# Optimization experiments

Hardware: AMD Instinct MI355X
Metric: run time of the kernel (lower is better)

The kernel has to match this reference:

```python
import jax, jax.numpy as jnp
import numpy as np

B, TQ, TK, D, NA = 8, 512, 2048, 1024, 512
H, HD = 16, 64          # n_head, head_dim (D = H*HD)
NE, HID = 4, 32         # n_experts, expert hidden_dim
EPS = 1e-6


def _rmsnorm(x, w):
    return x * jax.lax.rsqrt(jnp.mean(x * x, axis=-1, keepdims=True) + EPS) * w


def setup_inputs() -> dict:
    key = jax.random.key(0)
    ks = jax.random.split(key, 20)
    r = lambda i, shp: jax.random.normal(ks[i], shp, dtype=jnp.float32) * 0.02
    return {
        'q': jax.random.normal(ks[0], (B, TQ, D), dtype=jnp.float32),
        'kv': jax.random.normal(ks[1], (B, TK, D), dtype=jnp.float32),
        'qn_w': jnp.ones((D,), jnp.float32),
        'kva_w': jnp.ones((D,), jnp.float32),
        'kvi_w': jnp.ones((D,), jnp.float32),
        'dn_w': jnp.ones((D,), jnp.float32),
        'fn_w': jnp.ones((D,), jnp.float32),
        'Wq': r(2, (D, D)), 'bq': jnp.zeros((D,), jnp.float32),
        'Wk': r(3, (D, D)), 'bk': jnp.zeros((D,), jnp.float32),
        'Wv': r(4, (D, D)), 'bv': jnp.zeros((D,), jnp.float32),
        'Wo': r(5, (D, D)), 'bo': jnp.zeros((D,), jnp.float32),
        'active_bias': r(6, (D,)),
        'inactive_bias': r(7, (D,)),
        'log_temp': jnp.array(0.0, jnp.float32),
        'gate_attn': jnp.array(0.3, jnp.float32),
        'gate_ffn': jnp.array(0.7, jnp.float32),
        'Wr': r(8, (D, NE)), 'br': jnp.zeros((NE,), jnp.float32),
        'W1': r(9, (NE, D, 2 * HID)), 'b1': jnp.zeros((NE, 2 * HID), jnp.float32),
        'W2': r(10, (NE, HID, D)), 'b2': jnp.zeros((NE, D), jnp.float32),
        'kv_mask': jnp.ones((B, TK), bool),
        'n_actives': NA,
    }


def _forward(q, kv, qn_w, kva_w, kvi_w, dn_w, fn_w,
             Wq, bq, Wk, bk, Wv, bv, Wo, bo,
             active_bias, inactive_bias, log_temp, gate_attn, gate_ffn,
             Wr, br, W1, b1, W2, b2, kv_mask, n_actives):
    Na = int(n_actives)
    Tk = kv.shape[1]
    Ni = Tk - Na
    b, tq, d = q.shape

    # split-normed kv, with active/inactive learned biases injected pre-KV-proj
    kv_a = _rmsnorm(kv[:, :Na], kva_w) + active_bias
    kv_i = _rmsnorm(kv[:, Na:], kvi_w) + inactive_bias
    kv_b = jnp.concatenate([kv_a, kv_i], axis=1)

    qn = _rmsnorm(q, qn_w)
    qp = (qn @ Wq + bq).reshape(b, tq, H, HD).transpose(0, 2, 1, 3)  # (B,H,Tq,hd)
    k = (kv_b @ Wk + bk).reshape(b, Tk, H, HD).transpose(0, 2, 1, 3)
    v = (kv_b @ Wv + bv).reshape(b, Tk, H, HD).transpose(0, 2, 1, 3)

    # torch: q *= 1/sqrt(hd), then SDPA(q/temp, ...) applies another 1/sqrt(hd)
    temp = jnp.clip(jnp.exp(log_temp), 0.1, 10.0)
    scale = 1.0 / (HD * temp)

    def attn(kk, vv):
        logits = jnp.einsum('bhqd,bhkd->bhqk', qp, kk) * scale
        return jnp.einsum('bhqk,bhkd->bhqd', jax.nn.softmax(logits, axis=-1), vv)

    out = attn(k[:, :, :Na], v[:, :, :Na]) / np.sqrt(max(Na, 1)) \
        - attn(k[:, :, Na:], v[:, :, Na:]) / np.sqrt(max(Ni, 1))
    out = out.transpose(0, 2, 1, 3).reshape(b, tq, d)
    delta = _rmsnorm(out @ Wo + bo, dn_w)
    q_new = q + jax.nn.sigmoid(gate_attn) * delta

    # dense soft MoE over normed kv, with query-similarity logit bias
    x = _rmsnorm(kv, fn_w)
    logits = x @ Wr + br                                   # (B,Tk,NE)
    q_vec = jnp.mean(q_new, axis=1, keepdims=True)         # (B,1,D)
    sim = jnp.einsum('bqd,btd->bt', q_vec, x)              # (B,Tk)
    probs = jax.nn.softmax(logits + sim[..., None], axis=-1)

    h = jnp.einsum('btd,edh->bteh', x, W1) + b1            # (B,Tk,NE,2*HID)
    xp, g = h[..., :HID], h[..., HID:]
    act = xp * (g * jax.nn.sigmoid(g))                     # SwiGLU
    eo = jnp.einsum('bteh,ehd->bted', act, W2) + b2        # (B,Tk,NE,D)
    moe_out = jnp.einsum('bte,bted->btd', probs, eo)

    kv_new = kv + jax.nn.sigmoid(gate_ffn) * moe_out
    return q_new, kv_new


def reference(q, kv, qn_w, kva_w, kvi_w, dn_w, fn_w,
              Wq, bq, Wk, bk, Wv, bv, Wo, bo,
              active_bias, inactive_bias, log_temp, gate_attn, gate_ffn,
              Wr, br, W1, b1, W2, b2, kv_mask, n_actives):
    return _forward(q, kv, qn_w, kva_w, kvi_w, dn_w, fn_w,
                    Wq, bq, Wk, bk, Wv, bv, Wo, bo,
                    active_bias, inactive_bias, log_temp, gate_attn, gate_ffn,
                    Wr, br, W1, b1, W2, b2, kv_mask, n_actives)
```

## Files before the change

### kernel.cpp

```cpp
#include <hip/hip_runtime.h>
#include <hip/hip_bf16.h>
#include <stdint.h>


#define B_   8
#define TQ_  512
#define TK_  2048
#define D_   1024
#define H_   16
#define HD_  64
#define NE_  4
#define HID_ 32
#define EPSF 1e-6f
#define LOG2E 1.44269504f

typedef __bf16 bf16_t;
typedef __bf16 bf16x8 __attribute__((ext_vector_type(8)));
typedef __bf16 bf16x4 __attribute__((ext_vector_type(4)));
typedef float  f32x4  __attribute__((ext_vector_type(4)));

typedef __attribute__((address_space(1))) void gvoid_t;
typedef __attribute__((address_space(3))) void lvoid_t;

__device__ __forceinline__ void gld_lds16(const void* g, void* l) {
  __builtin_amdgcn_global_load_lds((gvoid_t*)g, (lvoid_t*)l, 16, 0, 0);
}

struct TP2 { const float* in[2]; bf16_t* out[2]; };

__global__ void transpose_conv2_kernel(TP2 p) {
  __shared__ float tile[32][33];
  const int bz = blockIdx.z;
  const float* in = p.in[bz];
  bf16_t* out = p.out[bz];
  const int rb = blockIdx.y * 32, cb = blockIdx.x * 32;
  const int txi = threadIdx.x, tyi = threadIdx.y;
#pragma unroll
  for (int i = 0; i < 32; i += 8)
    tile[tyi + i][txi] = in[(size_t)(rb + tyi + i) * D_ + cb + txi];
  __syncthreads();
#pragma unroll
  for (int i = 0; i < 32; i += 8)
    out[(size_t)(cb + tyi + i) * D_ + rb + txi] = (bf16_t)tile[txi][tyi + i];
}

__global__ void transpose_fragorder_kernel(TP2 p) {
  __shared__ float tile[32][33];
  const float* in = p.in[blockIdx.z];
  bf16_t* out = p.out[blockIdx.z];
  const int kb0 = blockIdx.y * 32;
  const int nb0 = blockIdx.x * 32;
  const int tx = threadIdx.x, ty = threadIdx.y;
#pragma unroll
  for (int i = 0; i < 32; i += 8)
    tile[ty + i][tx] = in[(size_t)(kb0 + ty + i) * D_ + nb0 + tx];
  __syncthreads();
  const int t = ty * 32 + tx;
  const int n_l = t >> 3;
  const int k_l = (t & 7) * 4;
  const int n = nb0 + n_l;
  const int k = kb0 + k_l;
  const int tile_n = n >> 7, rn = n & 127, hc = rn >> 6, rr = rn & 63;
  const int j = rr >> 4, l15 = rr & 15;
  const int s = k >> 5, lg = (k >> 3) & 3, e = k & 7;
  bf16x4 o;
#pragma unroll
  for (int c = 0; c < 4; ++c) o[c] = (bf16_t)tile[k_l + c][n_l];
  *(bf16x4*)&out[(size_t)tile_n * 131072 + s * 4096 + hc * 2048 +
                 j * 512 + (lg * 16 + l15) * 8 + e] = o;
}

__global__ void transpose_conv_kernel(const float* __restrict__ in, bf16_t* __restrict__ out,
                                      int R, int C, int in_bstride,
                                      int out_rstride, int ob_row, int ob_col) {
  __shared__ float tile[32][33];
  const int bz = blockIdx.z;
  const int rb = blockIdx.y * 32, cb = blockIdx.x * 32;
  const int txi = threadIdx.x, tyi = threadIdx.y;
  const float* inp = in + (size_t)bz * in_bstride;
#pragma unroll
  for (int i = 0; i < 32; i += 8) {
    const int r = rb + tyi + i, c = cb + txi;
    if (r < R && c < C) tile[tyi + i][txi] = inp[(size_t)r * C + c];
  }
  __syncthreads();
#pragma unroll
  for (int i = 0; i < 32; i += 8) {
    const int orow = cb + tyi + i;
    const int ocol = rb + txi;
    if (orow < C && ocol < R)
      out[(size_t)(orow + bz * ob_row) * out_rstride + bz * ob_col + ocol] =
          (bf16_t)tile[txi][tyi + i];
  }
}

__device__ __forceinline__ float block_rsum(float v, float* red) {
  v += __shfl_xor(v, 1);  v += __shfl_xor(v, 2);  v += __shfl_xor(v, 4);
  v += __shfl_xor(v, 8);  v += __shfl_xor(v, 16); v += __shfl_xor(v, 32);
  const int tid = threadIdx.x;
  if ((tid & 63) == 0) red[tid >> 6] = v;
  __syncthreads();
  return red[0] + red[1] + red[2] + red[3];
}

__global__ __launch_bounds__(256)
void rms_kv_kernel(const float* __restrict__ kv, const float* __restrict__ kva_w,
                   const float* __restrict__ kvi_w, const float* __restrict__ fn_w,
                   const float* __restrict__ ab, const float* __restrict__ ib,
                   const int* __restrict__ n_act, const float* __restrict__ Wr,
                   const float* __restrict__ br,
                   bf16_t* __restrict__ kvb, bf16_t* __restrict__ xn,
                   float* __restrict__ probs) {
  __shared__ float red[4];
  __shared__ f32x4 pred[4];
  const int row = blockIdx.x;
  const int t = row & (TK_ - 1);
  const int tid = threadIdx.x;
  const float* src = kv + (size_t)row * D_;
  f32x4 v = ((const f32x4*)src)[tid];
  float ss = v[0]*v[0] + v[1]*v[1] + v[2]*v[2] + v[3]*v[3];
  ss = block_rsum(ss, red);
  const float rs = rsqrtf(ss * (1.0f / D_) + EPSF);
  const int Na = n_act[0];
  const float* wsel = (t < Na) ? kva_w : kvi_w;
  const float* bsel = (t < Na) ? ab : ib;
  const int d = tid * 4;
  f32x4 wv = *(const f32x4*)(wsel + d);
  f32x4 bv = *(const f32x4*)(bsel + d);
  f32x4 fv = *(const f32x4*)(fn_w + d);
  bf16x4 o0, o1;
  f32x4 p4 = {};
#pragma unroll
  for (int c = 0; c < 4; ++c) {
    const float xv = v[c] * rs;
    const float xf = xv * fv[c];
    o0[c] = (bf16_t)(xv * wv[c] + bv[c]);
    o1[c] = (bf16_t)xf;
    const f32x4 w4 = *(const f32x4*)&Wr[(d + c) * 4];
    p4 += w4 * xf;
  }
  {
    const int rl = row & 127, hh = rl >> 6, rr2 = rl & 63;
    const int ii = rr2 >> 4, l15 = rr2 & 15;
    const int s2 = d >> 5, lg2 = (d >> 3) & 3, e2 = d & 7;
    *(bf16x4*)&kvb[(size_t)(row >> 7) * 131072 + s2 * 4096 + hh * 2048 +
                   ii * 512 + (lg2 * 16 + l15) * 8 + e2] = o0;
  }
  *(bf16x4*)&xn[(size_t)row * D_ + d] = o1;
#pragma unroll
  for (int m = 1; m <= 32; m <<= 1) {
    p4[0] += __shfl_xor(p4[0], m); p4[1] += __shfl_xor(p4[1], m);
    p4[2] += __shfl_xor(p4[2], m); p4[3] += __shfl_xor(p4[3], m);
  }
  if ((tid & 63) == 0) pred[tid >> 6] = p4;
  __syncthreads();
  if (tid == 0) {
    f32x4 s = pred[0] + pred[1] + pred[2] + pred[3];
    s[0] += br[0]; s[1] += br[1]; s[2] += br[2]; s[3] += br[3];
    const float mx = fmaxf(fmaxf(s[0], s[1]), fmaxf(s[2], s[3]));
    const float e0 = __expf(s[0] - mx), e1 = __expf(s[1] - mx);
    const float e2 = __expf(s[2] - mx), e3 = __expf(s[3] - mx);
    const float inv = 1.0f / (e0 + e1 + e2 + e3);
    f32x4 pr = { e0 * inv, e1 * inv, e2 * inv, e3 * inv };
    *(f32x4*)&probs[row * 4] = pr;
  }
}

__global__ __launch_bounds__(256)
void rms_q_kernel(const float* __restrict__ q, const float* __restrict__ qn_w,
                  bf16_t* __restrict__ qn) {
  __shared__ float red[4];
  const int row = blockIdx.x;
  const int tid = threadIdx.x;
  const float* src = q + (size_t)row * D_;
  f32x4 v = ((const f32x4*)src)[tid];
  float ss = v[0]*v[0] + v[1]*v[1] + v[2]*v[2] + v[3]*v[3];
  ss = block_rsum(ss, red);
  const float rs = rsqrtf(ss * (1.0f / D_) + EPSF);
  const int d = tid * 4;
  f32x4 wv = *(const f32x4*)(qn_w + d);
  bf16x4 o0;
#pragma unroll
  for (int c = 0; c < 4; ++c) o0[c] = (bf16_t)(v[c] * rs * wv[c]);
  *(bf16x4*)&qn[(size_t)row * D_ + d] = o0;
}

__device__ __forceinline__ int xcd_swz(int bx, int gx) {
  if ((gx & 7) == 0) { const int cpx = gx >> 3; return (bx & 7) * cpx + (bx >> 3); }
  return bx;
}

__global__ __launch_bounds__(256)
void gemm_kv(const bf16_t* __restrict__ A, const bf16_t* __restrict__ Wk,
             const bf16_t* __restrict__ Wv, const float* __restrict__ bk,
             const float* __restrict__ bv, bf16_t* __restrict__ Kout,
             bf16_t* __restrict__ Vt) {
  __shared__ alignas(16) bf16_t lds[3 * 12288];
  const int tid = threadIdx.x;
  const int lane = tid & 63;
  const int w = tid >> 6;
  const int wr = w >> 1, wc = w & 1;
  const int lane15 = lane & 15, lgrp = lane >> 4;

  const int flat = blockIdx.x;
  const int xcd = flat & 7;
  const int local = flat >> 3;
  const int tg = local >> 3;
  const int yy = local & 7;
  const int m0 = (xcd * 16 + tg) * 128;
  const int n0 = yy * 128;

  f32x4 acc_k[4][4] = {};
  f32x4 acc_v[4][4] = {};

  const bf16_t* ga = A  + (size_t)(m0 >> 7) * 131072 + tid * 8;
  const bf16_t* gk = Wk + (size_t)(n0 >> 7) * 131072 + tid * 8;
  const bf16_t* gv = Wv + (size_t)(n0 >> 7) * 131072 + tid * 8;

  auto STAGE = [&](int s) {
    bf16_t* dst = lds + (s % 3) * 12288 + tid * 8;
    const size_t so = (size_t)s * 4096;
    gld_lds16(ga + so,        dst);
    gld_lds16(ga + so + 2048, dst + 2048);
    gld_lds16(gk + so,        dst + 4096);
    gld_lds16(gk + so + 2048, dst + 6144);
    gld_lds16(gv + so,        dst + 8192);
    gld_lds16(gv + so + 2048, dst + 10240);
  };

  STAGE(0);
  STAGE(1);

  const int abase = wr * 2048 + lane * 8;
  const int bbase = wc * 2048 + lane * 8;
  for (int s = 0; s < 32; ++s) {
    if (s < 30) asm volatile("s_waitcnt vmcnt(6)" ::: "memory");
    else        asm volatile("s_waitcnt vmcnt(0)" ::: "memory");
    __builtin_amdgcn_s_barrier();
    __builtin_amdgcn_sched_barrier(0);
    const bf16_t* buf = lds + (s % 3) * 12288;
    bf16x8 af[4], bkf[4], bvf[4];
#pragma unroll
    for (int i = 0; i < 4; ++i) af[i]  = *(const bf16x8*)&buf[abase + i * 512];
#pragma unroll
    for (int j = 0; j < 4; ++j) bkf[j] = *(const bf16x8*)&buf[4096 + bbase + j * 512];
#pragma unroll
    for (int j = 0; j < 4; ++j) bvf[j] = *(const bf16x8*)&buf[8192 + bbase + j * 512];
    if (s + 2 < 32) STAGE(s + 2);
    __builtin_amdgcn_s_setprio(1);
#pragma unroll
    for (int i = 0; i < 4; ++i)
#pragma unroll
      for (int j = 0; j < 4; ++j) {
        acc_k[i][j] = __builtin_amdgcn_mfma_f32_16x16x32_bf16(af[i], bkf[j], acc_k[i][j], 0, 0, 0);
        acc_v[i][j] = __builtin_amdgcn_mfma_f32_16x16x32_bf16(af[i], bvf[j], acc_v[i][j], 0, 0, 0);
      }
    __builtin_amdgcn_s_setprio(0);
  }

  const int row0 = m0 + wr * 64 + (lgrp << 2);
  const int col0 = n0 + wc * 64 + lane15;
#pragma unroll
  for (int j = 0; j < 4; ++j) {
    const int cc = col0 + j * 16;
    const float bkv = bk[cc];
#pragma unroll
    for (int i = 0; i < 4; ++i) {
      const int rr = row0 + i * 16;
#pragma unroll
      for (int r = 0; r < 4; ++r)
        Kout[(size_t)(rr + r) * D_ + cc] = (bf16_t)(acc_k[i][j][r] + bkv);
    }
  }

  __syncthreads();
  bf16_t* vt_l = lds + w * 4608;
#pragma unroll
  for (int j = 0; j < 4; ++j) {
    const int nl = j * 16 + lane15;
    const float bvv = bv[n0 + wc * 64 + nl];
#pragma unroll
    for (int i = 0; i < 4; ++i) {
      bf16x4 pv;
#pragma unroll
      for (int r = 0; r < 4; ++r) pv[r] = (bf16_t)(acc_v[i][j][r] + bvv);
      *(bf16x4*)&vt_l[nl * 72 + i * 16 + lgrp * 4] = pv;
    }
  }
  const int bidx2 = m0 >> 11;
  const int tok0 = (m0 & (TK_ - 1)) + wr * 64;
  bf16_t* vbase = Vt + (size_t)bidx2 * D_ * TK_ + (size_t)(n0 + wc * 64) * TK_ + tok0;
#pragma unroll
  for (int it = 0; it < 8; ++it) {
    const int ln = (lane >> 3) + it * 8;
    const int tk = (lane & 7) * 8;
    const bf16x8 v8 = *(const bf16x8*)&vt_l[ln * 72 + tk];
    *(bf16x8*)&vbase[(size_t)ln * TK_ + tk] = v8;
  }
}

__device__ __forceinline__ void gemm_loop_db(const bf16_t* __restrict__ ga,
                                             const bf16_t* __restrict__ gb,
                                             bf16_t* As, bf16_t* Bs, int K,
                                             size_t rstep, int ar, int br2,
                                             int tid, f32x4 acc[4][4]) {
  gld_lds16(ga,         &As[tid * 8]);
  gld_lds16(ga + rstep, &As[2048 + tid * 8]);
  gld_lds16(gb,         &Bs[tid * 8]);
  gld_lds16(gb + rstep, &Bs[2048 + tid * 8]);
  int buf = 0;
  for (int k0 = 0; k0 < K; k0 += 32) {
    __syncthreads();
    if (k0 + 32 < K) {
      const int nb = buf ^ 1;
      gld_lds16(ga + k0 + 32,         &As[nb * 4096 + tid * 8]);
      gld_lds16(ga + k0 + 32 + rstep, &As[nb * 4096 + 2048 + tid * 8]);
      gld_lds16(gb + k0 + 32,         &Bs[nb * 4096 + tid * 8]);
      gld_lds16(gb + k0 + 32 + rstep, &Bs[nb * 4096 + 2048 + tid * 8]);
    }
    bf16x8 af[4], bfr[4];
#pragma unroll
    for (int i = 0; i < 4; ++i) af[i]  = *(const bf16x8*)&As[buf * 4096 + ar  + i * 512];
#pragma unroll
    for (int j = 0; j < 4; ++j) bfr[j] = *(const bf16x8*)&Bs[buf * 4096 + br2 + j * 512];
#pragma unroll
    for (int i = 0; i < 4; ++i)
#pragma unroll
      for (int j = 0; j < 4; ++j)
        acc[i][j] = __builtin_amdgcn_mfma_f32_16x16x32_bf16(af[i], bfr[j], acc[i][j], 0, 0, 0);
    buf ^= 1;
  }
}

__device__ __forceinline__ void gemm64_loop_db(const bf16_t* __restrict__ ga,
                                               const bf16_t* __restrict__ gb,
                                               bf16_t* As, bf16_t* Bs, int K,
                                               size_t rstep, int ar, int br2,
                                               int tid, f32x4 acc[2][4]) {
  gld_lds16(ga,         &As[tid * 8]);
  gld_lds16(gb,         &Bs[tid * 8]);
  gld_lds16(gb + rstep, &Bs[2048 + tid * 8]);
  int buf = 0;
  for (int k0 = 0; k0 < K; k0 += 32) {
    __syncthreads();
    if (k0 + 32 < K) {
      const int nb = buf ^ 1;
      gld_lds16(ga + k0 + 32,         &As[nb * 2048 + tid * 8]);
      gld_lds16(gb + k0 + 32,         &Bs[nb * 4096 + tid * 8]);
      gld_lds16(gb + k0 + 32 + rstep, &Bs[nb * 4096 + 2048 + tid * 8]);
    }
    bf16x8 af[2], bfr[4];
#pragma unroll
    for (int i = 0; i < 2; ++i) af[i]  = *(const bf16x8*)&As[buf * 2048 + ar  + i * 512];
#pragma unroll
    for (int j = 0; j < 4; ++j) bfr[j] = *(const bf16x8*)&Bs[buf * 4096 + br2 + j * 512];
#pragma unroll
    for (int i = 0; i < 2; ++i)
#pragma unroll
      for (int j = 0; j < 4; ++j)
        acc[i][j] = __builtin_amdgcn_mfma_f32_16x16x32_bf16(af[i], bfr[j], acc[i][j], 0, 0, 0);
    buf ^= 1;
  }
}

template<int HAS_BIAS>
__global__ __launch_bounds__(256)
void gemm64_tn(const bf16_t* __restrict__ A, const bf16_t* __restrict__ Wt,
               const float* __restrict__ bias, bf16_t* __restrict__ C,
               int M, int N, int K) {
  __shared__ alignas(16) bf16_t As[2 * 64 * 32];
  __shared__ alignas(16) bf16_t Bs[2 * 128 * 32];
  const int tid = threadIdx.x;
  const int lane = tid & 63;
  const int w = tid >> 6;
  const int wr = w >> 1, wc = w & 1;
  const int m0 = xcd_swz(blockIdx.x, gridDim.x) * 64;
  const int n0 = blockIdx.y * 128;

  f32x4 acc[2][4] = {};
  const bf16_t* ga = A  + (size_t)(m0 + (tid >> 2)) * K + (tid & 3) * 8;
  const bf16_t* gb = Wt + (size_t)(n0 + (tid >> 2)) * K + (tid & 3) * 8;
  const int kb = (lane >> 4) * 8;
  const int ar  = ((wr * 32 + (lane & 15)) << 5) + kb;
  const int br2 = ((wc * 64 + (lane & 15)) << 5) + kb;

  gemm64_loop_db(ga, gb, As, Bs, K, (size_t)64 * K, ar, br2, tid, acc);

  const int row0 = m0 + wr * 32 + ((lane >> 4) << 2);
  const int col0 = n0 + wc * 64 + (lane & 15);
#pragma unroll
  for (int j = 0; j < 4; ++j) {
    const int cc = col0 + j * 16;
    const float bv = HAS_BIAS ? bias[cc] : 0.0f;
#pragma unroll
    for (int i = 0; i < 2; ++i) {
      const int rr = row0 + i * 16;
#pragma unroll
      for (int r = 0; r < 4; ++r)
        C[(size_t)(rr + r) * N + cc] = (bf16_t)(acc[i][j][r] + bv);
    }
  }
}

__global__ __launch_bounds__(256)
void gemm64_h_act(const bf16_t* __restrict__ A, const bf16_t* __restrict__ Wt,
                  const float* __restrict__ bias, const float* __restrict__ probs,
                  bf16_t* __restrict__ a2) {
  __shared__ alignas(16) bf16_t As[2 * 64 * 32];
  __shared__ alignas(16) bf16_t Bs[2 * 128 * 32];
  const int K = D_;
  const int tid = threadIdx.x;
  const int lane = tid & 63;
  const int w = tid >> 6;
  const int wr = w >> 1, wc = w & 1;
  const int m0 = xcd_swz(blockIdx.x, gridDim.x) * 64;
  const int n0 = blockIdx.y * 128;

  f32x4 acc[2][4] = {};
  const bf16_t* ga = A  + (size_t)(m0 + (tid >> 2)) * K + (tid & 3) * 8;
  const bf16_t* gb = Wt + (size_t)(n0 + (tid >> 2)) * K + (tid & 3) * 8;
  const int kb = (lane >> 4) * 8;
  const int ar  = ((wr * 32 + (lane & 15)) << 5) + kb;
  const int br2 = ((wc * 64 + (lane & 15)) << 5) + kb;

  gemm64_loop_db(ga, gb, As, Bs, K, (size_t)64 * K, ar, br2, tid, acc);

  const int row0 = m0 + wr * 32 + ((lane >> 4) << 2);
  const int hbase = n0 + wc * 64 + (lane & 15);
  const int e = hbase >> 6;
#pragma unroll
  for (int j = 0; j < 2; ++j) {
    const int ch = hbase + j * 16;
    const float bx = bias[ch], bg = bias[ch + 32];
    const int ac = (ch & 63) + e * 32;
#pragma unroll
    for (int i = 0; i < 2; ++i) {
      const int rr = row0 + i * 16;
#pragma unroll
      for (int r = 0; r < 4; ++r) {
        const float xp = acc[i][j][r] + bx;
        const float g  = acc[i][j + 2][r] + bg;
        const float sg = 1.0f / (1.0f + __expf(-g));
        const float pr = probs[(size_t)(rr + r) * 4 + e];
        a2[(size_t)(rr + r) * 128 + ac] = (bf16_t)(pr * xp * g * sg);
      }
    }
  }
}

__global__ __launch_bounds__(256)
void gemm_moe_kvnew(const bf16_t* __restrict__ A, const bf16_t* __restrict__ Wt,
                    const float* __restrict__ kv, const float* __restrict__ probs,
                    const float* __restrict__ b2, const float* __restrict__ gate_ffn,
                    float* __restrict__ out) {
  __shared__ alignas(16) bf16_t As[2 * 128 * 32];
  __shared__ alignas(16) bf16_t Bs[2 * 128 * 32];
  const int K = 128, N = D_;
  const int tid = threadIdx.x;
  const int lane = tid & 63;
  const int w = tid >> 6;
  const int wr = w >> 1, wc = w & 1;
  const int m0 = xcd_swz(blockIdx.x, gridDim.x) * 128;
  const int n0 = blockIdx.y * 128;

  f32x4 acc[4][4] = {};
  const bf16_t* ga = A  + (size_t)(m0 + (tid >> 2)) * K + (tid & 3) * 8;
  const bf16_t* gb = Wt + (size_t)(n0 + (tid >> 2)) * K + (tid & 3) * 8;
  const int kb = (lane >> 4) * 8;
  const int ar  = ((wr * 64 + (lane & 15)) << 5) + kb;
  const int br2 = ((wc * 64 + (lane & 15)) << 5) + kb;

  gemm_loop_db(ga, gb, As, Bs, K, (size_t)64 * K, ar, br2, tid, acc);

  const float sgf = 1.0f / (1.0f + __expf(-gate_ffn[0]));
  const int row0 = m0 + wr * 64 + ((lane >> 4) << 2);
  const int col0 = n0 + wc * 64 + (lane & 15);
#pragma unroll
  for (int j = 0; j < 4; ++j) {
    const int cc = col0 + j * 16;
    const f32x4 b2v = { b2[0 * D_ + cc], b2[1 * D_ + cc], b2[2 * D_ + cc], b2[3 * D_ + cc] };
#pragma unroll
    for (int i = 0; i < 4; ++i) {
      const int rr = row0 + i * 16;
#pragma unroll
      for (int r = 0; r < 4; ++r) {
        const f32x4 pr = *(const f32x4*)&probs[(size_t)(rr + r) * 4];
        const float bsum = pr[0]*b2v[0] + pr[1]*b2v[1] + pr[2]*b2v[2] + pr[3]*b2v[3];
        out[(size_t)(rr + r) * N + cc] =
            kv[(size_t)(rr + r) * N + cc] + sgf * (acc[i][j][r] + bsum);
      }
    }
  }
}

__global__ __launch_bounds__(128, 2)
void attn_mfma_kernel(const bf16_t* __restrict__ qp, const bf16_t* __restrict__ kb,
                      const bf16_t* __restrict__ vt, bf16_t* __restrict__ attno,
                      const float* __restrict__ log_temp, const int* __restrict__ n_act) {
  __shared__ alignas(16) bf16_t Ks[2][64 * 64];
  __shared__ alignas(16) bf16_t Vs[2][64 * 64];
  __shared__ alignas(16) bf16_t Ps[2][32 * 64];

  const int dd = blockIdx.x;
  const int xcd = dd & 7, within = dd >> 3;
  const int qt = within & 7, slot0 = within >> 3;
  const int bh = slot0 * 8 + xcd;
  const int b = bh >> 4, h = bh & 15;

  const int tid = threadIdx.x;
  const int lane = tid & 63;
  const int w = tid >> 6;
  const int lane15 = lane & 15, lgrp = lane >> 4, l7 = lane & 7;
  const int Na = n_act[0];
  float temp = __expf(log_temp[0]);
  temp = fminf(fmaxf(temp, 0.1f), 10.0f);
  const float lsc = LOG2E / (64.0f * temp);
  const int rowbase = qt * 64 + w * 32;

  const bf16_t* qsrcA = qp + (size_t)(b * TQ_ + rowbase + lane15) * D_ + h * 64 + lgrp * 8;
  const bf16_t* qsrcB = qsrcA + (size_t)16 * D_;
  bf16x8 qfA0 = *(const bf16x8*)qsrcA;
  bf16x8 qfA1 = *(const bf16x8*)(qsrcA + 32);
  bf16x8 qfB0 = *(const bf16x8*)qsrcB;
  bf16x8 qfB1 = *(const bf16x8*)(qsrcB + 32);
#pragma unroll
  for (int j = 0; j < 8; ++j) {
    qfA0[j] = (bf16_t)((float)qfA0[j] * lsc);
    qfA1[j] = (bf16_t)((float)qfA1[j] * lsc);
    qfB0[j] = (bf16_t)((float)qfB0[j] * lsc);
    qfB1[j] = (bf16_t)((float)qfB1[j] * lsc);
  }

  const int srow = tid >> 3;
  const int schunk = (tid & 7) ^ (srow & 7);
  const bf16_t* ksrc = kb + (size_t)(b * TK_ + srow) * D_ + h * 64 + schunk * 8;
  const bf16_t* vsrc = vt + ((size_t)(b * 16 + h) * 64 + srow) * TK_ + schunk * 8;

  f32x4 oA[4] = {}, oB[4] = {}, outA[4] = {}, outB[4] = {};
  float laccA = 0.f, laccB = 0.f;

  const float inv_sa = rsqrtf((float)(Na > 1 ? Na : 1));
  const int Ni = TK_ - Na;
  const float inv_si = rsqrtf((float)(Ni > 1 ? Ni : 1));

#pragma unroll
  for (int r = 0; r < 4; ++r) {
    gld_lds16(ksrc + (size_t)r * 16 * D_, &Ks[0][r * 1024 + tid * 8]);
    gld_lds16(vsrc + (size_t)r * 16 * TK_, &Vs[0][r * 1024 + tid * 8]);
  }

  for (int t = 0; t < TK_ / 64; ++t) {
    const int cur = t & 1;
    __syncthreads();
    if (t + 1 < TK_ / 64) {
      const int nb = cur ^ 1;
      const bf16_t* kN = ksrc + (size_t)(t + 1) * 64 * D_;
      const bf16_t* vN = vsrc + (size_t)(t + 1) * 64;
#pragma unroll
      for (int r = 0; r < 4; ++r) {
        gld_lds16(kN + (size_t)r * 16 * D_, &Ks[nb][r * 1024 + tid * 8]);
        gld_lds16(vN + (size_t)r * 16 * TK_, &Vs[nb][r * 1024 + tid * 8]);
      }
    }

    f32x4 sA[4], sB[4];
    __builtin_amdgcn_s_setprio(1);
#pragma unroll
    for (int cf = 0; cf < 4; ++cf) {
      const int krow = (cf * 16 + lane15) * 64;
      const bf16x8 kf0 = *(const bf16x8*)&Ks[cur][krow + ((lgrp ^ l7) << 3)];
      const bf16x8 kf1 = *(const bf16x8*)&Ks[cur][krow + (((lgrp + 4) ^ l7) << 3)];
      f32x4 s = {};
      s = __builtin_amdgcn_mfma_f32_16x16x32_bf16(kf0, qfA0, s, 0, 0, 0);
      s = __builtin_amdgcn_mfma_f32_16x16x32_bf16(kf1, qfA1, s, 0, 0, 0);
      sA[cf] = s;
      f32x4 s2 = {};
      s2 = __builtin_amdgcn_mfma_f32_16x16x32_bf16(kf0, qfB0, s2, 0, 0, 0);
      s2 = __builtin_amdgcn_mfma_f32_16x16x32_bf16(kf1, qfB1, s2, 0, 0, 0);
      sB[cf] = s2;
    }
    __builtin_amdgcn_s_setprio(0);

#pragma unroll
    for (int cf = 0; cf < 4; ++cf) {
      const int c = cf * 2 + (lgrp >> 1);
      const int pcol = ((c ^ l7) << 3) + (lgrp & 1) * 4;
      f32x4 pA, pB;
#pragma unroll
      for (int r = 0; r < 4; ++r) pA[r] = exp2f(sA[cf][r]);
#pragma unroll
      for (int r = 0; r < 4; ++r) pB[r] = exp2f(sB[cf][r]);
      laccA += (pA[0] + pA[1]) + (pA[2] + pA[3]);
      laccB += (pB[0] + pB[1]) + (pB[2] + pB[3]);
      bf16x4 pvA, pvB;
#pragma unroll
      for (int r = 0; r < 4; ++r) { pvA[r] = (bf16_t)pA[r]; pvB[r] = (bf16_t)pB[r]; }
      *(bf16x4*)&Ps[w][lane15 * 64 + pcol]        = pvA;
      *(bf16x4*)&Ps[w][(16 + lane15) * 64 + pcol] = pvB;
    }

    {
      const int prowA = lane15 * 64;
      const int prowB = (16 + lane15) * 64;
      const bf16x8 paA0 = *(const bf16x8*)&Ps[w][prowA + ((lgrp ^ l7) << 3)];
      const bf16x8 paA1 = *(const bf16x8*)&Ps[w][prowA + (((lgrp + 4) ^ l7) << 3)];
      const bf16x8 paB0 = *(const bf16x8*)&Ps[w][prowB + ((lgrp ^ l7) << 3)];
      const bf16x8 paB1 = *(const bf16x8*)&Ps[w][prowB + (((lgrp + 4) ^ l7) << 3)];
      __builtin_amdgcn_s_setprio(1);
#pragma unroll
      for (int df = 0; df < 4; ++df) {
        const int vrow = (df * 16 + lane15) * 64;
        const bf16x8 vf0 = *(const bf16x8*)&Vs[cur][vrow + ((lgrp ^ l7) << 3)];
        const bf16x8 vf1 = *(const bf16x8*)&Vs[cur][vrow + (((lgrp + 4) ^ l7) << 3)];
        oA[df] = __builtin_amdgcn_mfma_f32_16x16x32_bf16(paA0, vf0, oA[df], 0, 0, 0);
        oA[df] = __builtin_amdgcn_mfma_f32_16x16x32_bf16(paA1, vf1, oA[df], 0, 0, 0);
        oB[df] = __builtin_amdgcn_mfma_f32_16x16x32_bf16(paB0, vf0, oB[df], 0, 0, 0);
        oB[df] = __builtin_amdgcn_mfma_f32_16x16x32_bf16(paB1, vf1, oB[df], 0, 0, 0);
      }
      __builtin_amdgcn_s_setprio(0);
    }

    const bool endA = ((t + 1) * 64 == Na);
    const bool endI = (t == TK_ / 64 - 1);
    if (endA || endI) {
      float lA = laccA, lB = laccB;
      lA += __shfl_xor(lA, 16); lA += __shfl_xor(lA, 32);
      lB += __shfl_xor(lB, 16); lB += __shfl_xor(lB, 32);
      const float ssc = endA ? inv_sa : -inv_si;
      f32x4 ivA, ivB;
#pragma unroll
      for (int r = 0; r < 4; ++r) {
        ivA[r] = ssc / __shfl(lA, lgrp * 4 + r);
        ivB[r] = ssc / __shfl(lB, lgrp * 4 + r);
      }
#pragma unroll
      for (int df = 0; df < 4; ++df) {
        outA[df] += oA[df] * ivA; oA[df] = (f32x4){};
        outB[df] += oB[df] * ivB; oB[df] = (f32x4){};
      }
      laccA = 0.f; laccB = 0.f;
    }
  }

#pragma unroll
  for (int df = 0; df < 4; ++df)
#pragma unroll
    for (int r = 0; r < 4; ++r) {
      const size_t ro = (size_t)(b * TQ_ + rowbase + lgrp * 4 + r) * D_ + h * 64 + df * 16 + lane15;
      attno[ro]           = (bf16_t)outA[df][r];
      attno[ro + 16 * D_] = (bf16_t)outB[df][r];
    }
}

__global__ __launch_bounds__(256)
void delta_qnew_kernel(const bf16_t* __restrict__ proj, const float* __restrict__ dn_w,
                       const float* __restrict__ q, const float* __restrict__ gate_attn,
                       float* __restrict__ qnew) {
  __shared__ float red[4];
  const int row = blockIdx.x;
  const int tid = threadIdx.x;
  bf16x4 pv = *(const bf16x4*)(proj + (size_t)row * D_ + tid * 4);
  f32x4 v;
#pragma unroll
  for (int c = 0; c < 4; ++c) v[c] = (float)pv[c];
  float ss = v[0]*v[0] + v[1]*v[1] + v[2]*v[2] + v[3]*v[3];
  ss = block_rsum(ss, red);
  const float rs = rsqrtf(ss * (1.0f / D_) + EPSF);
  const float sga = 1.0f / (1.0f + __expf(-gate_attn[0]));
  const int d = tid * 4;
  f32x4 wv = *(const f32x4*)(dn_w + d);
  f32x4 qv = *(const f32x4*)(q + (size_t)row * D_ + d);
  f32x4 out;
#pragma unroll
  for (int c = 0; c < 4; ++c) out[c] = qv[c] + sga * (v[c] * rs * wv[c]);
  *(f32x4*)&qnew[(size_t)row * D_ + d] = out;
}

extern "C" void kernel_launch(void* const* d_in, const int* in_sizes, int n_in,
                              void* d_out, int out_size, void* d_ws, size_t ws_size,
                              hipStream_t stream) {
  const float* q           = (const float*)d_in[0];
  const float* kv          = (const float*)d_in[1];
  const float* qn_w        = (const float*)d_in[2];
  const float* kva_w       = (const float*)d_in[3];
  const float* kvi_w       = (const float*)d_in[4];
  const float* dn_w        = (const float*)d_in[5];
  const float* fn_w        = (const float*)d_in[6];
  const float* Wq          = (const float*)d_in[7];
  const float* bq          = (const float*)d_in[8];
  const float* Wk          = (const float*)d_in[9];
  const float* bk          = (const float*)d_in[10];
  const float* Wv          = (const float*)d_in[11];
  const float* bv          = (const float*)d_in[12];
  const float* Wo          = (const float*)d_in[13];
  const float* bo          = (const float*)d_in[14];
  const float* active_bias = (const float*)d_in[15];
  const float* inactive_b  = (const float*)d_in[16];
  const float* log_temp    = (const float*)d_in[17];
  const float* gate_attn   = (const float*)d_in[18];
  const float* gate_ffn    = (const float*)d_in[19];
  const float* Wr          = (const float*)d_in[20];
  const float* br          = (const float*)d_in[21];
  const float* W1          = (const float*)d_in[22];
  const float* b1          = (const float*)d_in[23];
  const float* W2          = (const float*)d_in[24];
  const float* b2          = (const float*)d_in[25];
  const int*   n_act       = (const int*)d_in[27];

  char* ws = (char*)d_ws;
  size_t off = 0;
  auto alloc = [&](size_t bytes) -> char* {
    char* p = ws + off;
    off = (off + bytes + 255) & ~(size_t)255;
    return p;
  };

  bf16_t* wqT  = (bf16_t*)alloc((size_t)D_ * D_ * 2);
  bf16_t* wkT  = (bf16_t*)alloc((size_t)D_ * D_ * 2);
  bf16_t* wvT  = (bf16_t*)alloc((size_t)D_ * D_ * 2);
  bf16_t* woT  = (bf16_t*)alloc((size_t)D_ * D_ * 2);
  bf16_t* w1T  = (bf16_t*)alloc((size_t)256 * D_ * 2);
  bf16_t* w2T  = (bf16_t*)alloc((size_t)D_ * 128 * 2);
  bf16_t* kvb  = (bf16_t*)alloc((size_t)B_ * TK_ * D_ * 2);
  bf16_t* xn   = (bf16_t*)alloc((size_t)B_ * TK_ * D_ * 2);
  bf16_t* qn   = (bf16_t*)alloc((size_t)B_ * TQ_ * D_ * 2);
  bf16_t* qp   = (bf16_t*)alloc((size_t)B_ * TQ_ * D_ * 2);
  bf16_t* kbuf = (bf16_t*)alloc((size_t)B_ * TK_ * D_ * 2);
  bf16_t* vt   = (bf16_t*)alloc((size_t)B_ * D_ * TK_ * 2);
  float*  probs = (float*)alloc((size_t)B_ * TK_ * NE_ * 4);
  bf16_t* attno = qn;
  bf16_t* proj  = qp;
  bf16_t* a2buf = kbuf;
  (void)ws_size; (void)in_sizes; (void)n_in; (void)out_size;

  float* q_new_out  = (float*)d_out;
  float* kv_new_out = (float*)d_out + (size_t)B_ * TQ_ * D_;

  dim3 tb(32, 8);
  TP2 tpa; tpa.in[0] = Wq; tpa.in[1] = Wo; tpa.out[0] = wqT; tpa.out[1] = woT;
  transpose_conv2_kernel<<<dim3(32, 32, 2), tb, 0, stream>>>(tpa);
  TP2 tpf; tpf.in[0] = Wk; tpf.in[1] = Wv; tpf.out[0] = wkT; tpf.out[1] = wvT;
  transpose_fragorder_kernel<<<dim3(32, 32, 2), tb, 0, stream>>>(tpf);
  transpose_conv_kernel<<<dim3(2, 32, 4), tb, 0, stream>>>(W1, w1T, D_, 64, D_ * 64, D_, 64, 0);
  transpose_conv_kernel<<<dim3(32, 1, 4), tb, 0, stream>>>(W2, w2T, 32, D_, 32 * D_, 128, 0, 32);

  rms_kv_kernel<<<B_ * TK_, 256, 0, stream>>>(kv, kva_w, kvi_w, fn_w, active_bias,
                                              inactive_b, n_act, Wr, br, kvb, xn, probs);
  rms_q_kernel<<<B_ * TQ_, 256, 0, stream>>>(q, qn_w, qn);

  gemm64_tn<1><<<dim3(B_ * TQ_ / 64, D_ / 128), 256, 0, stream>>>(qn, wqT, bq, qp, B_ * TQ_, D_, D_);
  gemm_kv<<<B_ * TK_ / 128 * (D_ / 128), 256, 0, stream>>>(kvb, wkT, wvT, bk, bv, kbuf, vt);

  attn_mfma_kernel<<<B_ * H_ * (TQ_ / 64), 128, 0, stream>>>(qp, kbuf, vt, attno, log_temp, n_act);

  gemm64_tn<1><<<dim3(B_ * TQ_ / 64, D_ / 128), 256, 0, stream>>>(attno, woT, bo, proj, B_ * TQ_, D_, D_);
  delta_qnew_kernel<<<B_ * TQ_, 256, 0, stream>>>(proj, dn_w, q, gate_attn, q_new_out);

  gemm64_h_act<<<dim3(B_ * TK_ / 64, 2), 256, 0, stream>>>(xn, w1T, b1, probs, a2buf);
  gemm_moe_kvnew<<<dim3(B_ * TK_ / 128, D_ / 128), 256, 0, stream>>>(a2buf, w2T, kv, probs, b2,
                                                                     gate_ffn, kv_new_out);
}
```

Measured before the change: 330.4 us.

## Store GEMM operands in MFMA fragment order and use triple-buffered LDS pipelines

Producers (rms kernels, attention output, h_act epilogue, weight preprocessing) now write activations and weights directly in a fragment-tiled layout. The Q/O, W1 and MoE GEMMs can then stream contiguous 16-byte chunks into LDS through a three-stage global_load_lds pipeline with s_setprio around the MFMAs. This replaces the double-buffered row-major loaders and unifies the weight transpose kernels. The gemm_kv wait threshold is also loosened on the second-to-last iteration, which could race unless the outstanding-load count still holds there.

```diff
diff --git a/kernel.cpp b/kernel.cpp
--- a/kernel.cpp
+++ b/kernel.cpp
@@ -26,72 +26,40 @@
   __builtin_amdgcn_global_load_lds((gvoid_t*)g, (lvoid_t*)l, 16, 0, 0);
 }
 
-struct TP2 { const float* in[2]; bf16_t* out[2]; };
-
-__global__ void transpose_conv2_kernel(TP2 p) {
+__device__ __forceinline__ size_t frag64(int row, int d) {
+  return (size_t)(row >> 6) * 65536 + (size_t)(d >> 5) * 2048 +
+         ((row >> 5) & 1) * 1024 + ((row >> 4) & 1) * 512 +
+         ((((d >> 3) & 3) * 16 + (row & 15)) << 3) + (d & 7);
+}
+__device__ __forceinline__ size_t frag128k(int row, int k, int tns) {
+  return (size_t)(row >> 7) * tns + (size_t)(k >> 5) * 4096 +
+         ((row >> 6) & 1) * 2048 + ((row >> 4) & 3) * 512 +
+         ((((k >> 3) & 3) * 16 + (row & 15)) << 3) + (k & 7);
+}
+
+__global__ void fragorder_kernel(const float* __restrict__ in, bf16_t* __restrict__ out,
+                                 int C, int in_bstride, int obn, int obk, int tns) {
   __shared__ float tile[32][33];
   const int bz = blockIdx.z;
-  const float* in = p.in[bz];
-  bf16_t* out = p.out[bz];
+  const float* inp = in + (size_t)bz * in_bstride;
   const int rb = blockIdx.y * 32, cb = blockIdx.x * 32;
-  const int txi = threadIdx.x, tyi = threadIdx.y;
+  const int tx = threadIdx.x, ty = threadIdx.y;
 #pragma unroll
   for (int i = 0; i < 32; i += 8)
-    tile[tyi + i][txi] = in[(size_t)(rb + tyi + i) * D_ + cb + txi];
-  __syncthreads();
-#pragma unroll
-  for (int i = 0; i < 32; i += 8)
-    out[(size_t)(cb + tyi + i) * D_ + rb + txi] = (bf16_t)tile[txi][tyi + i];
-}
-
-__global__ void transpose_fragorder_kernel(TP2 p) {
-  __shared__ float tile[32][33];
-  const float* in = p.in[blockIdx.z];
-  bf16_t* out = p.out[blockIdx.z];
-  const int kb0 = blockIdx.y * 32;
-  const int nb0 = blockIdx.x * 32;
-  const int tx = threadIdx.x, ty = threadIdx.y;
-#pragma unroll
-  for (int i = 0; i < 32; i += 8)
-    tile[ty + i][tx] = in[(size_t)(kb0 + ty + i) * D_ + nb0 + tx];
+    tile[ty + i][tx] = inp[(size_t)(rb + ty + i) * C + cb + tx];
   __syncthreads();
   const int t = ty * 32 + tx;
   const int n_l = t >> 3;
   const int k_l = (t & 7) * 4;
-  const int n = nb0 + n_l;
-  const int k = kb0 + k_l;
-  const int tile_n = n >> 7, rn = n & 127, hc = rn >> 6, rr = rn & 63;
-  const int j = rr >> 4, l15 = rr & 15;
-  const int s = k >> 5, lg = (k >> 3) & 3, e = k & 7;
+  const int n = cb + n_l + bz * obn;
+  const int k = rb + k_l + bz * obk;
   bf16x4 o;
 #pragma unroll
   for (int c = 0; c < 4; ++c) o[c] = (bf16_t)tile[k_l + c][n_l];
-  *(bf16x4*)&out[(size_t)tile_n * 131072 + s * 4096 + hc * 2048 +
-                 j * 512 + (lg * 16 + l15) * 8 + e] = o;
-}
-
-__global__ void transpose_conv_kernel(const float* __restrict__ in, bf16_t* __restrict__ out,
-                                      int R, int C, int in_bstride,
-                                      int out_rstride, int ob_row, int ob_col) {
-  __shared__ float tile[32][33];
-  const int bz = blockIdx.z;
-  const int rb = blockIdx.y * 32, cb = blockIdx.x * 32;
-  const int txi = threadIdx.x, tyi = threadIdx.y;
-  const float* inp = in + (size_t)bz * in_bstride;
-#pragma unroll
-  for (int i = 0; i < 32; i += 8) {
-    const int r = rb + tyi + i, c = cb + txi;
-    if (r < R && c < C) tile[tyi + i][txi] = inp[(size_t)r * C + c];
-  }
-  __syncthreads();
-#pragma unroll
-  for (int i = 0; i < 32; i += 8) {
-    const int orow = cb + tyi + i;
-    const int ocol = rb + txi;
-    if (orow < C && ocol < R)
-      out[(size_t)(orow + bz * ob_row) * out_rstride + bz * ob_col + ocol] =
-          (bf16_t)tile[txi][tyi + i];
-  }
+  const size_t addr = (size_t)(n >> 7) * tns + (size_t)(k >> 5) * 4096 +
+                      ((n >> 6) & 1) * 2048 + ((n >> 4) & 3) * 512 +
+                      ((((k >> 3) & 3) * 16 + (n & 15)) << 3) + (k & 7);
+  *(bf16x4*)&out[addr] = o;
 }
 
 __device__ __forceinline__ float block_rsum(float v, float* red) {
@@ -139,14 +107,8 @@
     const f32x4 w4 = *(const f32x4*)&Wr[(d + c) * 4];
     p4 += w4 * xf;
   }
-  {
-    const int rl = row & 127, hh = rl >> 6, rr2 = rl & 63;
-    const int ii = rr2 >> 4, l15 = rr2 & 15;
-    const int s2 = d >> 5, lg2 = (d >> 3) & 3, e2 = d & 7;
-    *(bf16x4*)&kvb[(size_t)(row >> 7) * 131072 + s2 * 4096 + hh * 2048 +
-                   ii * 512 + (lg2 * 16 + l15) * 8 + e2] = o0;
-  }
-  *(bf16x4*)&xn[(size_t)row * D_ + d] = o1;
+  *(bf16x4*)&kvb[frag128k(row & (TK_ * 8 - 1), d, 131072) + (size_t)(row >> 7) * 0] = o0;
+  *(bf16x4*)&xn[frag64(row, d)] = o1;
 #pragma unroll
   for (int m = 1; m <= 32; m <<= 1) {
     p4[0] += __shfl_xor(p4[0], m); p4[1] += __shfl_xor(p4[1], m);
@@ -182,7 +144,7 @@
   bf16x4 o0;
 #pragma unroll
   for (int c = 0; c < 4; ++c) o0[c] = (bf16_t)(v[c] * rs * wv[c]);
-  *(bf16x4*)&qn[(size_t)row * D_ + d] = o0;
+  *(bf16x4*)&qn[frag64(row, d)] = o0;
 }
 
 __device__ __forceinline__ int xcd_swz(int bx, int gx) {
@@ -234,7 +196,7 @@
   const int abase = wr * 2048 + lane * 8;
   const int bbase = wc * 2048 + lane * 8;
   for (int s = 0; s < 32; ++s) {
-    if (s < 30) asm volatile("s_waitcnt vmcnt(6)" ::: "memory");
+    if (s < 31) asm volatile("s_waitcnt vmcnt(6)" ::: "memory");
     else        asm volatile("s_waitcnt vmcnt(0)" ::: "memory");
     __builtin_amdgcn_s_barrier();
     __builtin_amdgcn_sched_barrier(0);
@@ -299,93 +261,59 @@
   }
 }
 
-__device__ __forceinline__ void gemm_loop_db(const bf16_t* __restrict__ ga,
+__device__ __forceinline__ void gemm64p_loop(const bf16_t* __restrict__ ga,
                                              const bf16_t* __restrict__ gb,
-                                             bf16_t* As, bf16_t* Bs, int K,
-                                             size_t rstep, int ar, int br2,
-                                             int tid, f32x4 acc[4][4]) {
-  gld_lds16(ga,         &As[tid * 8]);
-  gld_lds16(ga + rstep, &As[2048 + tid * 8]);
-  gld_lds16(gb,         &Bs[tid * 8]);
-  gld_lds16(gb + rstep, &Bs[2048 + tid * 8]);
-  int buf = 0;
-  for (int k0 = 0; k0 < K; k0 += 32) {
-    __syncthreads();
-    if (k0 + 32 < K) {
-      const int nb = buf ^ 1;
-      gld_lds16(ga + k0 + 32,         &As[nb * 4096 + tid * 8]);
-      gld_lds16(ga + k0 + 32 + rstep, &As[nb * 4096 + 2048 + tid * 8]);
-      gld_lds16(gb + k0 + 32,         &Bs[nb * 4096 + tid * 8]);
-      gld_lds16(gb + k0 + 32 + rstep, &Bs[nb * 4096 + 2048 + tid * 8]);
-    }
-    bf16x8 af[4], bfr[4];
-#pragma unroll
-    for (int i = 0; i < 4; ++i) af[i]  = *(const bf16x8*)&As[buf * 4096 + ar  + i * 512];
-#pragma unroll
-    for (int j = 0; j < 4; ++j) bfr[j] = *(const bf16x8*)&Bs[buf * 4096 + br2 + j * 512];
-#pragma unroll
-    for (int i = 0; i < 4; ++i)
+                                             bf16_t* lds, int tid, int wr, int wc,
+                                             int lane, f32x4 acc[2][4]) {
+  auto STAGE = [&](int s) {
+    bf16_t* dst = lds + (s % 3) * 6144 + tid * 8;
+    const size_t so2 = (size_t)s * 2048;
+    const size_t so4 = (size_t)s * 4096;
+    gld_lds16(ga + so2,        dst);
+    gld_lds16(gb + so4,        dst + 2048);
+    gld_lds16(gb + so4 + 2048, dst + 4096);
+  };
+  STAGE(0);
+  STAGE(1);
+  const int abase = wr * 1024 + lane * 8;
+  const int bbase = 2048 + wc * 2048 + lane * 8;
+  for (int s = 0; s < 32; ++s) {
+    if (s < 31) asm volatile("s_waitcnt vmcnt(3)" ::: "memory");
+    else        asm volatile("s_waitcnt vmcnt(0)" ::: "memory");
+    __builtin_amdgcn_s_barrier();
+    __builtin_amdgcn_sched_barrier(0);
+    const bf16_t* buf = lds + (s % 3) * 6144;
+    bf16x8 af[2], bfr[4];
+#pragma unroll
+    for (int i = 0; i < 2; ++i) af[i]  = *(const bf16x8*)&buf[abase + i * 512];
+#pragma unroll
+    for (int j = 0; j < 4; ++j) bfr[j] = *(const bf16x8*)&buf[bbase + j * 512];
+    if (s + 2 < 32) STAGE(s + 2);
+    __builtin_amdgcn_s_setprio(1);
+#pragma unroll
+    for (int i = 0; i < 2; ++i)
 #pragma unroll
       for (int j = 0; j < 4; ++j)
         acc[i][j] = __builtin_amdgcn_mfma_f32_16x16x32_bf16(af[i], bfr[j], acc[i][j], 0, 0, 0);
-    buf ^= 1;
-  }
-}
-
-__device__ __forceinline__ void gemm64_loop_db(const bf16_t* __restrict__ ga,
-                                               const bf16_t* __restrict__ gb,
-                                               bf16_t* As, bf16_t* Bs, int K,
-                                               size_t rstep, int ar, int br2,
-                                               int tid, f32x4 acc[2][4]) {
-  gld_lds16(ga,         &As[tid * 8]);
-  gld_lds16(gb,         &Bs[tid * 8]);
-  gld_lds16(gb + rstep, &Bs[2048 + tid * 8]);
-  int buf = 0;
-  for (int k0 = 0; k0 < K; k0 += 32) {
-    __syncthreads();
-    if (k0 + 32 < K) {
-      const int nb = buf ^ 1;
-      gld_lds16(ga + k0 + 32,         &As[nb * 2048 + tid * 8]);
-      gld_lds16(gb + k0 + 32,         &Bs[nb * 4096 + tid * 8]);
-      gld_lds16(gb + k0 + 32 + rstep, &Bs[nb * 4096 + 2048 + tid * 8]);
-    }
-    bf16x8 af[2], bfr[4];
-#pragma unroll
-    for (int i = 0; i < 2; ++i) af[i]  = *(const bf16x8*)&As[buf * 2048 + ar  + i * 512];
-#pragma unroll
-    for (int j = 0; j < 4; ++j) bfr[j] = *(const bf16x8*)&Bs[buf * 4096 + br2 + j * 512];
-#pragma unroll
-    for (int i = 0; i < 2; ++i)
-#pragma unroll
-      for (int j = 0; j < 4; ++j)
-        acc[i][j] = __builtin_amdgcn_mfma_f32_16x16x32_bf16(af[i], bfr[j], acc[i][j], 0, 0, 0);
-    buf ^= 1;
+    __builtin_amdgcn_s_setprio(0);
   }
 }
 
 template<int HAS_BIAS>
 __global__ __launch_bounds__(256)
-void gemm64_tn(const bf16_t* __restrict__ A, const bf16_t* __restrict__ Wt,
-               const float* __restrict__ bias, bf16_t* __restrict__ C,
-               int M, int N, int K) {
-  __shared__ alignas(16) bf16_t As[2 * 64 * 32];
-  __shared__ alignas(16) bf16_t Bs[2 * 128 * 32];
+void gemm64p_tn(const bf16_t* __restrict__ A, const bf16_t* __restrict__ Wt,
+                const float* __restrict__ bias, bf16_t* __restrict__ C, int N) {
+  __shared__ alignas(16) bf16_t lds[3 * 6144];
   const int tid = threadIdx.x;
   const int lane = tid & 63;
   const int w = tid >> 6;
   const int wr = w >> 1, wc = w & 1;
   const int m0 = xcd_swz(blockIdx.x, gridDim.x) * 64;
   const int n0 = blockIdx.y * 128;
-
   f32x4 acc[2][4] = {};
-  const bf16_t* ga = A  + (size_t)(m0 + (tid >> 2)) * K + (tid & 3) * 8;
-  const bf16_t* gb = Wt + (size_t)(n0 + (tid >> 2)) * K + (tid & 3) * 8;
-  const int kb = (lane >> 4) * 8;
-  const int ar  = ((wr * 32 + (lane & 15)) << 5) + kb;
-  const int br2 = ((wc * 64 + (lane & 15)) << 5) + kb;
-
-  gemm64_loop_db(ga, gb, As, Bs, K, (size_t)64 * K, ar, br2, tid, acc);
-
+  const bf16_t* ga = A  + (size_t)(m0 >> 6) * 65536 + tid * 8;
+  const bf16_t* gb = Wt + (size_t)(n0 >> 7) * 131072 + tid * 8;
+  gemm64p_loop(ga, gb, lds, tid, wr, wc, lane, acc);
   const int row0 = m0 + wr * 32 + ((lane >> 4) << 2);
   const int col0 = n0 + wc * 64 + (lane & 15);
 #pragma unroll
@@ -403,28 +331,20 @@
 }
 
 __global__ __launch_bounds__(256)
-void gemm64_h_act(const bf16_t* __restrict__ A, const bf16_t* __restrict__ Wt,
-                  const float* __restrict__ bias, const float* __restrict__ probs,
-                  bf16_t* __restrict__ a2) {
-  __shared__ alignas(16) bf16_t As[2 * 64 * 32];
-  __shared__ alignas(16) bf16_t Bs[2 * 128 * 32];
-  const int K = D_;
+void gemm64p_h_act(const bf16_t* __restrict__ A, const bf16_t* __restrict__ Wt,
+                   const float* __restrict__ bias, const float* __restrict__ probs,
+                   bf16_t* __restrict__ a2) {
+  __shared__ alignas(16) bf16_t lds[3 * 6144];
   const int tid = threadIdx.x;
   const int lane = tid & 63;
   const int w = tid >> 6;
   const int wr = w >> 1, wc = w & 1;
   const int m0 = xcd_swz(blockIdx.x, gridDim.x) * 64;
   const int n0 = blockIdx.y * 128;
-
   f32x4 acc[2][4] = {};
-  const bf16_t* ga = A  + (size_t)(m0 + (tid >> 2)) * K + (tid & 3) * 8;
-  const bf16_t* gb = Wt + (size_t)(n0 + (tid >> 2)) * K + (tid & 3) * 8;
-  const int kb = (lane >> 4) * 8;
-  const int ar  = ((wr * 32 + (lane & 15)) << 5) + kb;
-  const int br2 = ((wc * 64 + (lane & 15)) << 5) + kb;
-
-  gemm64_loop_db(ga, gb, As, Bs, K, (size_t)64 * K, ar, br2, tid, acc);
-
+  const bf16_t* ga = A  + (size_t)(m0 >> 6) * 65536 + tid * 8;
+  const bf16_t* gb = Wt + (size_t)(n0 >> 7) * 131072 + tid * 8;
+  gemm64p_loop(ga, gb, lds, tid, wr, wc, lane, acc);
   const int row0 = m0 + wr * 32 + ((lane >> 4) << 2);
   const int hbase = n0 + wc * 64 + (lane & 15);
   const int e = hbase >> 6;
@@ -442,35 +362,60 @@
         const float g  = acc[i][j + 2][r] + bg;
         const float sg = 1.0f / (1.0f + __expf(-g));
         const float pr = probs[(size_t)(rr + r) * 4 + e];
-        a2[(size_t)(rr + r) * 128 + ac] = (bf16_t)(pr * xp * g * sg);
+        a2[frag128k(rr + r, ac, 16384)] = (bf16_t)(pr * xp * g * sg);
       }
     }
   }
 }
 
 __global__ __launch_bounds__(256)
-void gemm_moe_kvnew(const bf16_t* __restrict__ A, const bf16_t* __restrict__ Wt,
-                    const float* __restrict__ kv, const float* __restrict__ probs,
-                    const float* __restrict__ b2, const float* __restrict__ gate_ffn,
-                    float* __restrict__ out) {
-  __shared__ alignas(16) bf16_t As[2 * 128 * 32];
-  __shared__ alignas(16) bf16_t Bs[2 * 128 * 32];
-  const int K = 128, N = D_;
+void gemm_moe_p(const bf16_t* __restrict__ A, const bf16_t* __restrict__ Wt,
+                const float* __restrict__ kv, const float* __restrict__ probs,
+                const float* __restrict__ b2, const float* __restrict__ gate_ffn,
+                float* __restrict__ out) {
+  __shared__ alignas(16) bf16_t lds[3 * 8192];
+  const int N = D_;
   const int tid = threadIdx.x;
   const int lane = tid & 63;
   const int w = tid >> 6;
   const int wr = w >> 1, wc = w & 1;
   const int m0 = xcd_swz(blockIdx.x, gridDim.x) * 128;
   const int n0 = blockIdx.y * 128;
-
   f32x4 acc[4][4] = {};
-  const bf16_t* ga = A  + (size_t)(m0 + (tid >> 2)) * K + (tid & 3) * 8;
-  const bf16_t* gb = Wt + (size_t)(n0 + (tid >> 2)) * K + (tid & 3) * 8;
-  const int kb = (lane >> 4) * 8;
-  const int ar  = ((wr * 64 + (lane & 15)) << 5) + kb;
-  const int br2 = ((wc * 64 + (lane & 15)) << 5) + kb;
-
-  gemm_loop_db(ga, gb, As, Bs, K, (size_t)64 * K, ar, br2, tid, acc);
+  const bf16_t* ga = A  + (size_t)(m0 >> 7) * 16384 + tid * 8;
+  const bf16_t* gb = Wt + (size_t)(n0 >> 7) * 16384 + tid * 8;
+  auto STAGE = [&](int s) {
+    bf16_t* dst = lds + (s % 3) * 8192 + tid * 8;
+    const size_t so = (size_t)s * 4096;
+    gld_lds16(ga + so,        dst);
+    gld_lds16(ga + so + 2048, dst + 2048);
+    gld_lds16(gb + so,        dst + 4096);
+    gld_lds16(gb + so + 2048, dst + 6144);
+  };
+  STAGE(0);
+  STAGE(1);
+  const int abase = wr * 2048 + lane * 8;
+  const int bbase = 4096 + wc * 2048 + lane * 8;
+  for (int s = 0; s < 4; ++s) {
+    if (s < 3) asm volatile("s_waitcnt vmcnt(4)" ::: "memory");
+    else       asm volatile("s_waitcnt vmcnt(0)" ::: "memory");
+    __builtin_amdgcn_s_barrier();
+    __builtin_amdgcn_sched_barrier(0);
+    const bf16_t* buf = lds + (s % 3) * 8192;
+    bf16x8 af[4], bfr[4];
+#pragma unroll
+    for (int i = 0; i < 4; ++i) af[i]  = *(const bf16x8*)&buf[abase + i * 512];
+#pragma unroll
+    for (int j = 0; j < 4; ++j) bfr[j] = *(const bf16x8*)&buf[bbase + j * 512];
+    if (s + 2 < 4) STAGE(s + 2);
+    __builtin_amdgcn_s_setprio(1);
+#pragma unroll
+    for (int i = 0; i < 4; ++i)
+#pragma unroll
+      for (int j = 0; j < 4; ++j)
+        acc[i][j] = __builtin_amdgcn_mfma_f32_16x16x32_bf16(af[i], bfr[j], acc[i][j], 0, 0, 0);
+    __builtin_amdgcn_s_setprio(0);
+  }
 
   const float sgf = 1.0f / (1.0f + __expf(-gate_ffn[0]));
   const int row0 = m0 + wr * 64 + ((lane >> 4) << 2);
@@ -646,9 +591,10 @@
   for (int df = 0; df < 4; ++df)
 #pragma unroll
     for (int r = 0; r < 4; ++r) {
-      const size_t ro = (size_t)(b * TQ_ + rowbase + lgrp * 4 + r) * D_ + h * 64 + df * 16 + lane15;
-      attno[ro]           = (bf16_t)outA[df][r];
-      attno[ro + 16 * D_] = (bf16_t)outB[df][r];
+      const int Rr = b * TQ_ + rowbase + lgrp * 4 + r;
+      const int col = h * 64 + df * 16 + lane15;
+      attno[frag64(Rr, col)]      = (bf16_t)outA[df][r];
+      attno[frag64(Rr + 16, col)] = (bf16_t)outB[df][r];
     }
 }
 
@@ -737,26 +683,26 @@
   float* kv_new_out = (float*)d_out + (size_t)B_ * TQ_ * D_;
 
   dim3 tb(32, 8);
-  TP2 tpa; tpa.in[0] = Wq; tpa.in[1] = Wo; tpa.out[0] = wqT; tpa.out[1] = woT;
-  transpose_conv2_kernel<<<dim3(32, 32, 2), tb, 0, stream>>>(tpa);
-  TP2 tpf; tpf.in[0] = Wk; tpf.in[1] = Wv; tpf.out[0] = wkT; tpf.out[1] = wvT;
-  transpose_fragorder_kernel<<<dim3(32, 32, 2), tb, 0, stream>>>(tpf);
-  transpose_conv_kernel<<<dim3(2, 32, 4), tb, 0, stream>>>(W1, w1T, D_, 64, D_ * 64, D_, 64, 0);
-  transpose_conv_kernel<<<dim3(32, 1, 4), tb, 0, stream>>>(W2, w2T, 32, D_, 32 * D_, 128, 0, 32);
+  fragorder_kernel<<<dim3(32, 32, 1), tb, 0, stream>>>(Wq, wqT, D_, 0, 0, 0, 131072);
+  fragorder_kernel<<<dim3(32, 32, 1), tb, 0, stream>>>(Wk, wkT, D_, 0, 0, 0, 131072);
+  fragorder_kernel<<<dim3(32, 32, 1), tb, 0, stream>>>(Wv, wvT, D_, 0, 0, 0, 131072);
+  fragorder_kernel<<<dim3(32, 32, 1), tb, 0, stream>>>(Wo, woT, D_, 0, 0, 0, 131072);
+  fragorder_kernel<<<dim3(2, 32, 4), tb, 0, stream>>>(W1, w1T, 64, D_ * 64, 64, 0, 131072);
+  fragorder_kernel<<<dim3(32, 1, 4), tb, 0, stream>>>(W2, w2T, D_, 32 * D_, 0, 32, 16384);
 
   rms_kv_kernel<<<B_ * TK_, 256, 0, stream>>>(kv, kva_w, kvi_w, fn_w, active_bias,
                                               inactive_b, n_act, Wr, br, kvb, xn, probs);
   rms_q_kernel<<<B_ * TQ_, 256, 0, stream>>>(q, qn_w, qn);
 
-  gemm64_tn<1><<<dim3(B_ * TQ_ / 64, D_ / 128), 256, 0, stream>>>(qn, wqT, bq, qp, B_ * TQ_, D_, D_);
+  gemm64p_tn<1><<<dim3(B_ * TQ_ / 64, D_ / 128), 256, 0, stream>>>(qn, wqT, bq, qp, D_);
   gemm_kv<<<B_ * TK_ / 128 * (D_ / 128), 256, 0, stream>>>(kvb, wkT, wvT, bk, bv, kbuf, vt);
 
   attn_mfma_kernel<<<B_ * H_ * (TQ_ / 64), 128, 0, stream>>>(qp, kbuf, vt, attno, log_temp, n_act);
 
-  gemm64_tn<1><<<dim3(B_ * TQ_ / 64, D_ / 128), 256, 0, stream>>>(attno, woT, bo, proj, B_ * TQ_, D_, D_);
+  gemm64p_tn<1><<<dim3(B_ * TQ_ / 64, D_ / 128), 256, 0, stream>>>(attno, woT, bo, proj, D_);
   delta_qnew_kernel<<<B_ * TQ_, 256, 0, stream>>>(proj, dn_w, q, gate_attn, q_new_out);
 
-  gemm64_h_act<<<dim3(B_ * TK_ / 64, 2), 256, 0, stream>>>(xn, w1T, b1, probs, a2buf);
-  gemm_moe_kvnew<<<dim3(B_ * TK_ / 128, D_ / 128), 256, 0, stream>>>(a2buf, w2T, kv, probs, b2,
-                                                                     gate_ffn, kv_new_out);
-}
+  gemm64p_h_act<<<dim3(B_ * TK_ / 64, 2), 256, 0, stream>>>(xn, w1T, b1, probs, a2buf);
+  gemm_moe_p<<<dim3(B_ * TK_ / 128, D_ / 128), 256, 0, stream>>>(a2buf, w2T, kv, probs, b2,
+                                                                 gate_ffn, kv_new_out);
+}
```

After: 358.2 us. 1.08x slower.
